# Kernel tuning notes

Hardware: AMD Instinct MI355X
Metric: run time of the kernel (lower is better)

Reference implementation:

```python
import jax, jax.numpy as jnp
import numpy as np

EPS = 1e-6  # F.normalize eps

N, C, H, W = 2, 64, 64, 64
HEADS, DK, DV = 2, 64, 32


def setup_inputs() -> dict:
    key = jax.random.key(0)
    ks = jax.random.split(key, 9)
    w = lambda k, sh: jax.random.normal(k, sh, jnp.float32) * 0.05
    return {
        "x":  jax.random.normal(ks[0], (N, C, H, W), jnp.float32),
        "Wq": w(ks[1], (HEADS, DK, C)), "bq": w(ks[2], (HEADS, DK)),
        "Wk": w(ks[3], (HEADS, DK, C)), "bk": w(ks[4], (HEADS, DK)),
        "Wv": w(ks[5], (HEADS, DV, C)), "bv": w(ks[6], (HEADS, DV)),
        "Wm": w(ks[7], (C, HEADS * DV)), "bm": w(ks[8], (C,)),
    }


def _l2norm(t):
    # F.normalize(dim=1) on [N, dk, L]; here heads are stacked: [N, h, dk, L], axis=2
    n = jnp.linalg.norm(t, axis=2, keepdims=True)
    return t / jnp.maximum(n, EPS)


def reference(x, Wq, bq, Wk, bk, Wv, bv, Wm, bm):
    n, c, h, w = x.shape
    L = h * w
    xf = x.reshape(n, c, L)  # 1x1 conv == pointwise channel GEMM; x_enc = x (no pos enc)
    Q = jnp.einsum('hkc,ncl->nhkl', Wq, xf) + bq[None, :, :, None]
    K = jnp.einsum('hkc,ncl->nhkl', Wk, xf) + bk[None, :, :, None]
    V = jnp.einsum('hvc,ncl->nhvl', Wv, xf) + bv[None, :, :, None]
    Q = _l2norm(Q)
    K = _l2norm(K)
    # cosine-similarity attention: contract over dk, softmax over keys
    A = jax.nn.softmax(jnp.einsum('nhkl,nhkm->nhlm', Q, K), axis=-1)  # [n,h,L,L]
    R = jnp.einsum('nhlm,nhvm->nhvl', A, V)  # [n,h,dv,L]
    Rc = R.reshape(n, -1, L)  # concat heads along channels
    out = jnp.einsum('oc,ncl->nol', Wm, Rc) + bm[None, :, None]
    return out.reshape(n, c, h, w) + x  # residual
```

## Files before the change

kernel.cpp:

```cpp
#include <hip/hip_runtime.h>
#include <cmath>


typedef __bf16 bf16x8 __attribute__((ext_vector_type(8)));
typedef __bf16 bf16x4 __attribute__((ext_vector_type(4)));
typedef float f4_t __attribute__((ext_vector_type(4)));

#define LQ 4096
#define NH 4
#define KS 8

__device__ inline f4_t mfma16(bf16x8 a, bf16x8 b, f4_t c) {
    return __builtin_amdgcn_mfma_f32_16x16x32_bf16(a, b, c, 0, 0, 0);
}

__global__ void k0_prep(const float* __restrict__ Wq, const float* __restrict__ bq,
                        const float* __restrict__ Wk, const float* __restrict__ bk,
                        const float* __restrict__ Wv, const float* __restrict__ bv,
                        __bf16* __restrict__ Wb, float* __restrict__ bb) {
    const int tid = threadIdx.x;
    const int row = blockIdx.x * 64 + (tid >> 2);
    const int c0  = (tid & 3) * 16;

    const float* wsrc;
    float bval;
    if (row < 128)      { wsrc = Wq + (size_t)row * 64;         bval = bq[row]; }
    else if (row < 256) { wsrc = Wk + (size_t)(row - 128) * 64; bval = bk[row - 128]; }
    else                { wsrc = Wv + (size_t)(row - 256) * 64; bval = bv[row - 256]; }

#pragma unroll
    for (int j = 0; j < 16; ++j)
        Wb[(size_t)row * 64 + c0 + j] = (__bf16)wsrc[c0 + j];
    if ((tid & 3) == 0) bb[row] = bval;
}

__global__ __launch_bounds__(256) void k1_qkv(
        const float* __restrict__ x,
        const __bf16* __restrict__ Wb, const float* __restrict__ bb,
        __bf16* __restrict__ Qb, __bf16* __restrict__ Kb,
        __bf16* __restrict__ Vtb) {
    const int tid  = threadIdx.x;
    const int lane = tid & 63;
    const int w    = tid >> 6;
    const int quad = lane >> 4;
    const int l15  = lane & 15;
    const int lt   = blockIdx.x;
    const int n    = blockIdx.y;
    const int l0   = lt * 32;

    __shared__ __bf16 xl[32][72];

    {
        const int c0 = tid >> 5, l = tid & 31;
#pragma unroll
        for (int i = 0; i < 8; ++i) {
            const int c = c0 + i * 8;
            xl[l][c] = (__bf16)x[((size_t)n * 64 + c) * LQ + l0 + l];
        }
    }

    bf16x8 af[4][2], av[2];
#pragma unroll
    for (int t = 0; t < 4; ++t)
#pragma unroll
        for (int kh = 0; kh < 2; ++kh)
            af[t][kh] = *(const bf16x8*)(Wb +
                (size_t)(w * 64 + t * 16 + l15) * 64 + kh * 32 + quad * 8);
#pragma unroll
    for (int kh = 0; kh < 2; ++kh)
        av[kh] = *(const bf16x8*)(Wb +
            (size_t)(256 + w * 16 + l15) * 64 + kh * 32 + quad * 8);

    f4_t binit[4], bvinit;
#pragma unroll
    for (int t = 0; t < 4; ++t)
#pragma unroll
        for (int r = 0; r < 4; ++r)
            binit[t][r] = bb[w * 64 + t * 16 + quad * 4 + r];
#pragma unroll
    for (int r = 0; r < 4; ++r)
        bvinit[r] = bb[256 + w * 16 + quad * 4 + r];

    __syncthreads();

    f4_t acc[4][2], vacc[2];
#pragma unroll
    for (int lsub = 0; lsub < 2; ++lsub) {
        bf16x8 bf0 = *(const bf16x8*)&xl[lsub * 16 + l15][quad * 8];
        bf16x8 bf1 = *(const bf16x8*)&xl[lsub * 16 + l15][32 + quad * 8];
#pragma unroll
        for (int t = 0; t < 4; ++t) {
            f4_t a = mfma16(af[t][0], bf0, binit[t]);
            acc[t][lsub] = mfma16(af[t][1], bf1, a);
        }
        f4_t va = mfma16(av[0], bf0, bvinit);
        vacc[lsub] = mfma16(av[1], bf1, va);
    }

    const int nh = n * 2 + (w & 1);
    __bf16* dst  = (w < 2) ? Qb : Kb;
#pragma unroll
    for (int lsub = 0; lsub < 2; ++lsub) {
        float ss = 0.f;
#pragma unroll
        for (int t = 0; t < 4; ++t)
#pragma unroll
            for (int r = 0; r < 4; ++r)
                ss = fmaf(acc[t][lsub][r], acc[t][lsub][r], ss);
        ss += __shfl_xor(ss, 16, 64);
        ss += __shfl_xor(ss, 32, 64);
        const float rn = 1.0f / fmaxf(sqrtf(ss), 1e-6f);

        const int l = l0 + lsub * 16 + l15;
#pragma unroll
        for (int t = 0; t < 4; ++t) {
            bf16x4 pk;
#pragma unroll
            for (int r = 0; r < 4; ++r) pk[r] = (__bf16)(acc[t][lsub][r] * rn);
            const int kc = t * 2 + (quad >> 1);
            *(bf16x4*)(dst + ((size_t)(nh * 8 + kc) * LQ + l) * 8 + (quad & 1) * 4) = pk;
        }
#pragma unroll
        for (int r = 0; r < 4; ++r) {
            const int vrow = w * 16 + quad * 4 + r;
            Vtb[(size_t)(n * 64 + vrow) * LQ + l] = (__bf16)vacc[lsub][r];
        }
    }
}

__global__ __launch_bounds__(256, 4) void k2_attn(
        const __bf16* __restrict__ Qb, const __bf16* __restrict__ Kb,
        const __bf16* __restrict__ Vtb,
        float* __restrict__ numP, float* __restrict__ denP) {
    const int tid  = threadIdx.x;
    const int lane = tid & 63;
    const int wave = tid >> 6;
    const int quad = lane >> 4;
    const int l15  = lane & 15;
    const int nh   = blockIdx.y;
    const int ks   = blockIdx.z;
    const int qbase = blockIdx.x * 128 + wave * 32;
    const int kbase = ks * 512;

    __shared__ __bf16 Kl[2][2048];
    __shared__ __bf16 P[4][2][16][40];

    const f4_t fzero = {0.f, 0.f, 0.f, 0.f};

    const int s_kc = ((tid >> 6) & 1) * 4 + ((tid >> 4) & 3);
    const int s_l  = ((tid >> 7) << 4) | (tid & 15);
    const __bf16* s_src = Kb + ((size_t)(nh * 8 + s_kc) * LQ + kbase + s_l) * 8;

    bf16x8 qf[2][2];
#pragma unroll
    for (int qt = 0; qt < 2; ++qt)
#pragma unroll
        for (int kh = 0; kh < 2; ++kh)
            qf[qt][kh] = *(const bf16x8*)(Qb +
                ((size_t)(nh * 8 + kh * 4 + quad) * LQ + qbase + qt * 16 + l15) * 8);

    f4_t racc[2][2];
#pragma unroll
    for (int a = 0; a < 2; ++a)
#pragma unroll
        for (int b = 0; b < 2; ++b) racc[a][b] = fzero;
    float den[2] = {0.f, 0.f};

    *(bf16x8*)&Kl[0][tid * 8] = *(const bf16x8*)s_src;
    __syncthreads();

    for (int ch = 0; ch < 16; ++ch) {
        const int cur = ch & 1;

        if (ch < 15)
            *(bf16x8*)&Kl[cur ^ 1][tid * 8] =
                *(const bf16x8*)(s_src + (size_t)(ch + 1) * 32 * 8);

        const int kb = kbase + ch * 32;

        bf16x8 vf[2];
#pragma unroll
        for (int vt = 0; vt < 2; ++vt)
            vf[vt] = *(const bf16x8*)(Vtb +
                (size_t)(nh * 32 + vt * 16 + l15) * LQ + kb + quad * 8);

        bf16x8 kf[2][2];
#pragma unroll
        for (int kt = 0; kt < 2; ++kt)
#pragma unroll
            for (int kh = 0; kh < 2; ++kh)
                kf[kt][kh] = *(const bf16x8*)
                    &Kl[cur][(kt * 128 + kh * 64 + quad * 16 + l15) * 8];

        f4_t s[2][2];
#pragma unroll
        for (int qt = 0; qt < 2; ++qt)
#pragma unroll
            for (int kt = 0; kt < 2; ++kt) {
                f4_t t = mfma16(kf[kt][0], qf[qt][0], fzero);
                s[qt][kt] = mfma16(kf[kt][1], qf[qt][1], t);
            }

#pragma unroll
        for (int qt = 0; qt < 2; ++qt)
#pragma unroll
            for (int kt = 0; kt < 2; ++kt) {
                bf16x4 pv;
                float d = 0.f;
#pragma unroll
                for (int r = 0; r < 4; ++r) {
                    float p = __expf(s[qt][kt][r]);
                    d += p;
                    pv[r] = (__bf16)p;
                }
                den[qt] += d;
                *(bf16x4*)&P[wave][qt][l15][kt * 16 + quad * 4] = pv;
            }

#pragma unroll
        for (int qt = 0; qt < 2; ++qt) {
            bf16x8 pf = *(const bf16x8*)&P[wave][qt][l15][quad * 8];
#pragma unroll
            for (int vt = 0; vt < 2; ++vt)
                racc[vt][qt] = mfma16(vf[vt], pf, racc[vt][qt]);
        }

        __syncthreads();
    }

#pragma unroll
    for (int qt = 0; qt < 2; ++qt) {
        den[qt] += __shfl_xor(den[qt], 16, 64);
        den[qt] += __shfl_xor(den[qt], 32, 64);
    }

    const size_t pb = (size_t)(nh * KS + ks) * LQ;
#pragma unroll
    for (int vt = 0; vt < 2; ++vt)
#pragma unroll
        for (int qt = 0; qt < 2; ++qt)
#pragma unroll
            for (int r = 0; r < 4; ++r)
                numP[(pb + qbase + qt * 16 + l15) * 32 + vt * 16 + quad * 4 + r]
                    = racc[vt][qt][r];

    if (lane < 16)
#pragma unroll
        for (int qt = 0; qt < 2; ++qt)
            denP[pb + qbase + qt * 16 + lane] = den[qt];
}

__global__ __launch_bounds__(256) void k3_out(
        const float* __restrict__ numP, const float* __restrict__ denP,
        const float* __restrict__ Wm, const float* __restrict__ bm,
        const float* __restrict__ x, float* __restrict__ out) {
    const int tid  = threadIdx.x;
    const int lane = tid & 63;
    const int wv   = tid >> 6;
    const int n    = blockIdx.x >> 6;
    const int lt   = blockIdx.x & 63;
    const int l0   = lt * 64;

    __shared__ float Rf[64][65];
    __shared__ float dinv[2][64];

    if (tid < 128) {
        const int hh = tid >> 6, li = tid & 63;
        float s = 0.f;
#pragma unroll
        for (int k = 0; k < KS; ++k)
            s += denP[(size_t)((n * 2 + hh) * KS + k) * LQ + l0 + li];
        dinv[hh][li] = 1.0f / s;
    }

    {
        const int v = tid & 31, lsub = tid >> 5;
#pragma unroll
        for (int hh = 0; hh < 2; ++hh) {
            const size_t base = (size_t)(n * 2 + hh) * KS * LQ;
#pragma unroll
            for (int i = 0; i < 8; ++i) {
                const int l = lsub + 8 * i;
                float s = 0.f;
#pragma unroll
                for (int k = 0; k < KS; ++k)
                    s += numP[(base + (size_t)k * LQ + l0 + l) * 32 + v];
                Rf[hh * 32 + v][l] = s;
            }
        }
    }
    __syncthreads();

    const float d0 = dinv[0][lane], d1 = dinv[1][lane];
    float rj[64];
#pragma unroll
    for (int j = 0; j < 64; ++j)
        rj[j] = Rf[j][lane] * (j < 32 ? d0 : d1);

    float acc[16];
#pragma unroll
    for (int oi = 0; oi < 16; ++oi) acc[oi] = bm[wv * 16 + oi];
#pragma unroll
    for (int oi = 0; oi < 16; ++oi) {
        const float* wr = Wm + (size_t)(wv * 16 + oi) * 64;
        float a = acc[oi];
#pragma unroll
        for (int j4 = 0; j4 < 16; ++j4) {
            f4_t t = *(const f4_t*)(wr + j4 * 4);
            a = fmaf(t[0], rj[j4 * 4 + 0], a);
            a = fmaf(t[1], rj[j4 * 4 + 1], a);
            a = fmaf(t[2], rj[j4 * 4 + 2], a);
            a = fmaf(t[3], rj[j4 * 4 + 3], a);
        }
        acc[oi] = a;
    }

#pragma unroll
    for (int oi = 0; oi < 16; ++oi) {
        const int o = wv * 16 + oi;
        const size_t idx = (size_t)(n * 64 + o) * LQ + l0 + lane;
        out[idx] = acc[oi] + x[idx];
    }
}

extern "C" void kernel_launch(void* const* d_in, const int* in_sizes, int n_in,
                              void* d_out, int out_size, void* d_ws, size_t ws_size,
                              hipStream_t stream) {
    const float* x  = (const float*)d_in[0];
    const float* Wq = (const float*)d_in[1];
    const float* bq = (const float*)d_in[2];
    const float* Wk = (const float*)d_in[3];
    const float* bk = (const float*)d_in[4];
    const float* Wv = (const float*)d_in[5];
    const float* bv = (const float*)d_in[6];
    const float* Wm = (const float*)d_in[7];
    const float* bm = (const float*)d_in[8];
    float* out = (float*)d_out;

    __bf16* Qb  = (__bf16*)d_ws;
    __bf16* Kb  = Qb + (size_t)NH * LQ * 64;
    __bf16* Vtb = Kb + (size_t)NH * LQ * 64;
    float*  numP = (float*)(Vtb + (size_t)NH * 32 * LQ);
    float*  denP = numP + (size_t)NH * KS * 32 * LQ;
    __bf16* Wb  = (__bf16*)(denP + (size_t)NH * KS * LQ);
    float*  bb  = (float*)(Wb + 320 * 64);

    k0_prep<<<dim3(5), dim3(256), 0, stream>>>(Wq, bq, Wk, bk, Wv, bv, Wb, bb);
    k1_qkv<<<dim3(128, 2), dim3(256), 0, stream>>>(x, Wb, bb, Qb, Kb, Vtb);
    k2_attn<<<dim3(32, NH, KS), dim3(256), 0, stream>>>(Qb, Kb, Vtb, numP, denP);
    k3_out<<<dim3(128), dim3(256), 0, stream>>>(numP, denP, Wm, bm, x, out);
}
```

Baseline: 120.6 us.

## Fold log2e into Q normalization and feed P to PV MFMA directly from registers

Scales the normalized Q by log2(e) in the projection kernel so the attention loop can use exp2 instead of exp. When a 16x16x16 bf16 MFMA builtin is available, the P tile stays in registers and feeds that instruction directly, dropping the shared-memory round trip for P. The V fragments are loaded as 4-wide pieces to match that layout. The cost is twice as many smaller-K MFMAs for the PV product, and the result depends on which builtin the compiler exposes.

New measurement: 135.2 us. 1.12x slower.

```diff
diff --git a/kernel.cpp b/kernel.cpp
--- a/kernel.cpp
+++ b/kernel.cpp
@@ -4,6 +4,7 @@
 
 typedef __bf16 bf16x8 __attribute__((ext_vector_type(8)));
 typedef __bf16 bf16x4 __attribute__((ext_vector_type(4)));
+typedef short short4_t __attribute__((ext_vector_type(4)));
 typedef float f4_t __attribute__((ext_vector_type(4)));
 
 #define LQ 4096
@@ -13,6 +14,21 @@
 __device__ inline f4_t mfma16(bf16x8 a, bf16x8 b, f4_t c) {
     return __builtin_amdgcn_mfma_f32_16x16x32_bf16(a, b, c, 0, 0, 0);
 }
+
+#if __has_builtin(__builtin_amdgcn_mfma_f32_16x16x16_bf16)
+#define HAVE_PV16 1
+__device__ inline f4_t pv_mfma(bf16x4 a, bf16x4 b, f4_t c) {
+    return __builtin_amdgcn_mfma_f32_16x16x16_bf16(a, b, c, 0, 0, 0);
+}
+#elif __has_builtin(__builtin_amdgcn_mfma_f32_16x16x16bf16_1k)
+#define HAVE_PV16 1
+__device__ inline f4_t pv_mfma(bf16x4 a, bf16x4 b, f4_t c) {
+    return __builtin_amdgcn_mfma_f32_16x16x16bf16_1k(
+        __builtin_bit_cast(short4_t, a), __builtin_bit_cast(short4_t, b), c, 0, 0, 0);
+}
+#else
+#define HAVE_PV16 0
+#endif
 
 __global__ void k0_prep(const float* __restrict__ Wq, const float* __restrict__ bq,
                         const float* __restrict__ Wk, const float* __restrict__ bk,
@@ -99,6 +115,7 @@
 
     const int nh = n * 2 + (w & 1);
     __bf16* dst  = (w < 2) ? Qb : Kb;
+    const float post = (w < 2) ? 1.44269504f : 1.0f;
 #pragma unroll
     for (int lsub = 0; lsub < 2; ++lsub) {
         float ss = 0.f;
@@ -109,7 +126,7 @@
                 ss = fmaf(acc[t][lsub][r], acc[t][lsub][r], ss);
         ss += __shfl_xor(ss, 16, 64);
         ss += __shfl_xor(ss, 32, 64);
-        const float rn = 1.0f / fmaxf(sqrtf(ss), 1e-6f);
+        const float rn = post / fmaxf(sqrtf(ss), 1e-6f);
 
         const int l = l0 + lsub * 16 + l15;
 #pragma unroll
@@ -143,7 +160,9 @@
     const int kbase = ks * 512;
 
     __shared__ __bf16 Kl[2][2048];
+#if !HAVE_PV16
     __shared__ __bf16 P[4][2][16][40];
+#endif
 
     const f4_t fzero = {0.f, 0.f, 0.f, 0.f};
 
@@ -177,12 +196,6 @@
                 *(const bf16x8*)(s_src + (size_t)(ch + 1) * 32 * 8);
 
         const int kb = kbase + ch * 32;
-
-        bf16x8 vf[2];
-#pragma unroll
-        for (int vt = 0; vt < 2; ++vt)
-            vf[vt] = *(const bf16x8*)(Vtb +
-                (size_t)(nh * 32 + vt * 16 + l15) * LQ + kb + quad * 8);
 
         bf16x8 kf[2][2];
 #pragma unroll
@@ -201,22 +214,58 @@
                 s[qt][kt] = mfma16(kf[kt][1], qf[qt][1], t);
             }
 
+#if HAVE_PV16
+        bf16x4 vf4[2][2];
+#pragma unroll
+        for (int vt = 0; vt < 2; ++vt)
+#pragma unroll
+            for (int kt = 0; kt < 2; ++kt)
+                vf4[vt][kt] = *(const bf16x4*)(Vtb +
+                    (size_t)(nh * 32 + vt * 16 + l15) * LQ + kb + kt * 16 + quad * 4);
+
+        bf16x4 pv[2][2];
 #pragma unroll
         for (int qt = 0; qt < 2; ++qt)
 #pragma unroll
             for (int kt = 0; kt < 2; ++kt) {
-                bf16x4 pv;
                 float d = 0.f;
 #pragma unroll
                 for (int r = 0; r < 4; ++r) {
-                    float p = __expf(s[qt][kt][r]);
+                    float p = __builtin_exp2f(s[qt][kt][r]);
                     d += p;
-                    pv[r] = (__bf16)p;
+                    pv[qt][kt][r] = (__bf16)p;
                 }
                 den[qt] += d;
-                *(bf16x4*)&P[wave][qt][l15][kt * 16 + quad * 4] = pv;
             }
 
+#pragma unroll
+        for (int qt = 0; qt < 2; ++qt)
+#pragma unroll
+            for (int kt = 0; kt < 2; ++kt)
+#pragma unroll
+                for (int vt = 0; vt < 2; ++vt)
+                    racc[vt][qt] = pv_mfma(vf4[vt][kt], pv[qt][kt], racc[vt][qt]);
+#else
+        bf16x8 vf[2];
+#pragma unroll
+        for (int vt = 0; vt < 2; ++vt)
+            vf[vt] = *(const bf16x8*)(Vtb +
+                (size_t)(nh * 32 + vt * 16 + l15) * LQ + kb + quad * 8);
+#pragma unroll
+        for (int qt = 0; qt < 2; ++qt)
+#pragma unroll
+            for (int kt = 0; kt < 2; ++kt) {
+                bf16x4 pvv;
+                float d = 0.f;
+#pragma unroll
+                for (int r = 0; r < 4; ++r) {
+                    float p = __builtin_exp2f(s[qt][kt][r]);
+                    d += p;
+                    pvv[r] = (__bf16)p;
+                }
+                den[qt] += d;
+                *(bf16x4*)&P[wave][qt][l15][kt * 16 + quad * 4] = pvv;
+            }
 #pragma unroll
         for (int qt = 0; qt < 2; ++qt) {
             bf16x8 pf = *(const bf16x8*)&P[wave][qt][l15][quad * 8];
@@ -224,6 +273,7 @@
             for (int vt = 0; vt < 2; ++vt)
                 racc[vt][qt] = mfma16(vf[vt], pf, racc[vt][qt]);
         }
+#endif
 
         __syncthreads();
     }
```
